# Kernel optimization log

Measured on AMD Instinct MI355X. Metric: run time of the kernel, lower is better.

The kernel has to match this reference:

```python
import jax, jax.numpy as jnp
import numpy as np

B, L, D_IN = 4, 2048, 80
D, H, DFF, WIN = 128, 16, 128, 64
DH = D // H
BN_EPS = 1e-5


def sinusoidal_positional_encoding(l, d, dtype):
    # Faithful to source: pos_j = 10000 ** (j / d) (exponent j/d, not 2j/d)
    n = d // 2 + (d % 2 == 1)
    pos_i = jnp.arange(l, dtype=dtype)[:, None]                  # [L,1]
    pos_j = jnp.power(jnp.asarray(10000.0, dtype), jnp.arange(n, dtype=dtype) / d)  # [n]
    ang = pos_i / pos_j                                          # [L,n]
    pos = jnp.stack([jnp.sin(ang), jnp.cos(ang)], axis=-1).reshape(l, -1)
    return pos[:, :d]                                            # [L,D]


def local_window_disallowed_mask(l, win):
    # Source: mask starts as ones (True = disallowed), zeros only strictly
    i = jnp.arange(l)
    diff = jnp.abs(i[:, None] - i[None, :])
    allowed = (diff >= 1) & (diff <= win)
    return ~allowed                                              # [L,L] bool, True = masked


def setup_inputs() -> dict:
    key = jax.random.key(0)
    ks = jax.random.split(key, 17)
    s = 0.05  # weight scale for numerical stability
    return {
        "x": jax.random.normal(ks[0], (B, L, D_IN), jnp.float32),
        "conv_w": jax.random.normal(ks[1], (D, D_IN), jnp.float32) * s,
        "conv_b": jax.random.normal(ks[2], (D,), jnp.float32) * s,
        "bn_g": jax.random.uniform(ks[3], (D,), jnp.float32, 0.5, 1.5),
        "bn_b": jax.random.normal(ks[4], (D,), jnp.float32) * s,
        "bn_rm": jax.random.normal(ks[5], (D,), jnp.float32) * s,
        "bn_rv": jax.random.uniform(ks[6], (D,), jnp.float32, 0.5, 1.5),
        "in_proj_w": jax.random.normal(ks[7], (3 * D, D), jnp.float32) * s,
        "in_proj_b": jax.random.normal(ks[8], (3 * D,), jnp.float32) * s,
        "out_w": jax.random.normal(ks[9], (D, D), jnp.float32) * s,
        "out_b": jax.random.normal(ks[10], (D,), jnp.float32) * s,
        "ff_w1": jax.random.normal(ks[11], (DFF, D), jnp.float32) * s,
        "ff_b1": jax.random.normal(ks[12], (DFF,), jnp.float32) * s,
        "ff_w2": jax.random.normal(ks[13], (D, DFF), jnp.float32) * s,
        "ff_b2": jax.random.normal(ks[14], (D,), jnp.float32) * s,
        "fc_w": jax.random.normal(ks[15], (D_IN, D), jnp.float32) * s,
        "fc_b": jax.random.normal(ks[16], (D_IN,), jnp.float32) * s,
    }


def _forward(x, conv_w, conv_b, bn_g, bn_b, bn_rm, bn_rv,
             in_proj_w, in_proj_b, out_w, out_b,
             ff_w1, ff_b1, ff_w2, ff_b2, fc_w, fc_b):
    b, l, _ = x.shape
    dt = x.dtype
    # Conv1d(kernel=1) + ReLU + BatchNorm1d (eval mode, running stats)
    h = jax.nn.relu(jnp.einsum('bli,oi->blo', x, conv_w) + conv_b)     # [B,L,D]
    h = (h - bn_rm) * (bn_g * jax.lax.rsqrt(bn_rv + BN_EPS)) + bn_b
    # positional encoding
    h = h + sinusoidal_positional_encoding(l, D, dt)
    # MultiheadAttention (torch semantics: joint in_proj, scaled dot, out_proj)
    qkv = jnp.einsum('bld,ed->ble', h, in_proj_w) + in_proj_b          # [B,L,3D]
    q, k, v = jnp.split(qkv, 3, axis=-1)
    q = q.reshape(b, l, H, DH).transpose(0, 2, 1, 3)                   # [B,H,L,dh]
    k = k.reshape(b, l, H, DH).transpose(0, 2, 1, 3)
    v = v.reshape(b, l, H, DH).transpose(0, 2, 1, 3)
    scores = jnp.einsum('bhqd,bhkd->bhqk', q, k) / jnp.sqrt(jnp.asarray(DH, dt))
    mask = local_window_disallowed_mask(l, WIN)                        # True = masked
    scores = jnp.where(mask, jnp.finfo(dt).min, scores)
    attn = jax.nn.softmax(scores, axis=-1)                             # [B,H,L,L]
    ctx = jnp.einsum('bhqk,bhkd->bhqd', attn, v)
    ctx = ctx.transpose(0, 2, 1, 3).reshape(b, l, D)
    attn_out = jnp.einsum('bld,od->blo', ctx, out_w) + out_b           # [B,L,D]
    # FFN (no residual in source)
    f = jax.nn.relu(jnp.einsum('bld,fd->blf', attn_out, ff_w1) + ff_b1)
    f = jnp.einsum('blf,df->bld', f, ff_w2) + ff_b2                    # [B,L,D]
    # final head
    return jnp.einsum('bld,od->blo', f, fc_w) + fc_b                   # [B,L,80]


def reference(x, conv_w, conv_b, bn_g, bn_b, bn_rm, bn_rv,
              in_proj_w, in_proj_b, out_w, out_b,
              ff_w1, ff_b1, ff_w2, ff_b2, fc_w, fc_b):
    return _forward(x, conv_w, conv_b, bn_g, bn_b, bn_rm, bn_rv,
                    in_proj_w, in_proj_b, out_w, out_b,
                    ff_w1, ff_b1, ff_w2, ff_b2, fc_w, fc_b)
```

## Files before the change

### kernel.cpp

```cpp
#include <hip/hip_runtime.h>
#include <math.h>

constexpr int L_ = 2048, D_ = 128, H_ = 16;
constexpr int T_ = 8192;
constexpr int LDX = T_;

typedef __attribute__((ext_vector_type(8))) short short8;
typedef __attribute__((ext_vector_type(4))) float floatx4;

__device__ unsigned short g_h_hi[T_ * D_];
__device__ unsigned short g_h_lo[T_ * D_];
__device__ unsigned short g_Wq_hi[3 * D_ * D_];
__device__ unsigned short g_Wq_lo[3 * D_ * D_];
__device__ float g_qkv [3 * D_ * T_];
__device__ unsigned short g_ctxH[T_ * D_];
__device__ unsigned short g_ctxL[T_ * D_];
__device__ unsigned short g_Mf1H[D_ * D_];
__device__ unsigned short g_Mf1L[D_ * D_];
__device__ unsigned short g_MfcH[D_ * D_];
__device__ unsigned short g_MfcL[D_ * D_];
__device__ float g_bf1 [D_];
__device__ float g_bfc [D_];

__device__ __forceinline__ unsigned short bf16h(float x) {
    unsigned u = __float_as_uint(x);
    return (unsigned short)((u + 0x7FFFu + ((u >> 16) & 1u)) >> 16);
}
__device__ __forceinline__ float bf16f(unsigned short h) {
    return __uint_as_float(((unsigned)h) << 16);
}

__global__ __launch_bounds__(256) void stage1_kernel(
        const float* __restrict__ x, const float* __restrict__ conv_w,
        const float* __restrict__ conv_b,
        const float* __restrict__ bg, const float* __restrict__ bb,
        const float* __restrict__ brm, const float* __restrict__ brv,
        const float* __restrict__ in_proj_w,
        const float* __restrict__ out_w,  const float* __restrict__ out_b,
        const float* __restrict__ ff_w1,  const float* __restrict__ ff_b1,
        const float* __restrict__ ff_w2,  const float* __restrict__ ff_b2,
        const float* __restrict__ fc_w,   const float* __restrict__ fc_b) {
    __shared__ unsigned short sm[2 * 32 * 104];
    int bid = blockIdx.x, tid = threadIdx.x;

    if (bid < 256) {
        unsigned short* XsH = sm;
        unsigned short* XsL = sm + 32 * 104;
        int t0 = bid * 32;

        for (int p = tid; p < 1280; p += 256) {
            int f0 = p * 2;
            int r = f0 / 80, k = f0 - r * 80;
            float2 v2 = *(const float2*)&x[(size_t)(t0 + r) * 80 + k];
            unsigned short h0 = bf16h(v2.x), h1 = bf16h(v2.y);
            *(unsigned*)&XsH[r * 104 + k] = (unsigned)h0 | ((unsigned)h1 << 16);
            *(unsigned*)&XsL[r * 104 + k] =
                (unsigned)bf16h(v2.x - bf16f(h0)) |
                ((unsigned)bf16h(v2.y - bf16f(h1)) << 16);
        }
        for (int i = tid; i < 384; i += 256) {
            int r = i / 12, k = 80 + 2 * (i - r * 12);
            *(unsigned*)&XsH[r * 104 + k] = 0u;
            *(unsigned*)&XsL[r * 104 + k] = 0u;
        }
        __syncthreads();

        int lane = tid & 63, w = tid >> 6;
        int m16 = lane & 15, quad = lane >> 4;

        short8 aH[2][3], aL[2][3];
#pragma unroll
        for (int mt = 0; mt < 2; mt++) {
            int c = w * 32 + mt * 16 + m16;
#pragma unroll
            for (int kt = 0; kt < 3; kt++) {
                int kb = kt * 32 + quad * 8;
                short8 vh = {0, 0, 0, 0, 0, 0, 0, 0};
                short8 vl = {0, 0, 0, 0, 0, 0, 0, 0};
                if (kb < 80) {
                    float4 f0 = *(const float4*)&conv_w[(size_t)c * 80 + kb];
                    float4 f1 = *(const float4*)&conv_w[(size_t)c * 80 + kb + 4];
                    float vv[8] = {f0.x, f0.y, f0.z, f0.w, f1.x, f1.y, f1.z, f1.w};
#pragma unroll
                    for (int e = 0; e < 8; e++) {
                        unsigned short hh = bf16h(vv[e]);
                        vh[e] = (short)hh;
                        vl[e] = (short)bf16h(vv[e] - bf16f(hh));
                    }
                }
                aH[mt][kt] = vh; aL[mt][kt] = vl;
            }
        }

#pragma unroll
        for (int mt = 0; mt < 2; mt++) {
#pragma unroll
            for (int nt = 0; nt < 2; nt++) {
                floatx4 acc = {0.f, 0.f, 0.f, 0.f};
                int trow = nt * 16 + m16;
#pragma unroll
                for (int kt = 0; kt < 3; kt++) {
                    short8 bHv = *(short8*)&XsH[trow * 104 + kt * 32 + quad * 8];
                    short8 bLv = *(short8*)&XsL[trow * 104 + kt * 32 + quad * 8];
                    acc = __builtin_amdgcn_mfma_f32_16x16x32_bf16(aH[mt][kt], bHv, acc, 0, 0, 0);
                    acc = __builtin_amdgcn_mfma_f32_16x16x32_bf16(aL[mt][kt], bHv, acc, 0, 0, 0);
                    acc = __builtin_amdgcn_mfma_f32_16x16x32_bf16(aH[mt][kt], bLv, acc, 0, 0, 0);
                }
                int c0 = w * 32 + mt * 16 + quad * 4;
                int t = t0 + nt * 16 + m16;
                int l = t & 2047;
                float vr[4];
#pragma unroll
                for (int r = 0; r < 4; r++) {
                    int c = c0 + r;
                    float v = acc[r] + conv_b[c];
                    v = fmaxf(v, 0.0f);
                    v = (v - brm[c]) * (bg[c] * rsqrtf(brv[c] + 1e-5f)) + bb[c];
                    float inv = __expf((float)(c >> 1) * (-9.210340371976184f / 128.0f));
                    float ang = (float)l * inv;
                    v += (c & 1) ? cosf(ang) : sinf(ang);
                    vr[r] = v;
                }
                unsigned short h0 = bf16h(vr[0]), h1 = bf16h(vr[1]);
                unsigned short h2 = bf16h(vr[2]), h3 = bf16h(vr[3]);
                unsigned hp[2] = {(unsigned)h0 | ((unsigned)h1 << 16),
                                  (unsigned)h2 | ((unsigned)h3 << 16)};
                unsigned lp[2] = {
                    (unsigned)bf16h(vr[0] - bf16f(h0)) | ((unsigned)bf16h(vr[1] - bf16f(h1)) << 16),
                    (unsigned)bf16h(vr[2] - bf16f(h2)) | ((unsigned)bf16h(vr[3] - bf16f(h3)) << 16)};
                *(uint2*)&g_h_hi[(size_t)t * 128 + c0] = *(uint2*)hp;
                *(uint2*)&g_h_lo[(size_t)t * 128 + c0] = *(uint2*)lp;
            }
        }
        return;
    }
    if (bid < 304) {
        int e4 = ((bid - 256) * 256 + tid) * 4;
        float4 v = *(const float4*)&in_proj_w[e4];
        float vv[4] = {v.x, v.y, v.z, v.w};
        unsigned short hh[4], ll[4];
#pragma unroll
        for (int e = 0; e < 4; e++) {
            hh[e] = bf16h(vv[e]);
            ll[e] = bf16h(vv[e] - bf16f(hh[e]));
        }
        unsigned hp[2] = {(unsigned)hh[0] | ((unsigned)hh[1] << 16),
                          (unsigned)hh[2] | ((unsigned)hh[3] << 16)};
        unsigned lp[2] = {(unsigned)ll[0] | ((unsigned)ll[1] << 16),
                          (unsigned)ll[2] | ((unsigned)ll[3] << 16)};
        *(uint2*)&g_Wq_hi[e4] = *(uint2*)hp;
        *(uint2*)&g_Wq_lo[e4] = *(uint2*)lp;
        return;
    }
    float* rowbuf = (float*)sm;
    float* red = (float*)sm + 256;
    if (bid < 368) {
        int sub = tid >> 7, k = tid & 127;
        int f = (bid - 304) * 2 + sub;
        rowbuf[sub * 128 + k] = ff_w1[f * 128 + k];
        __syncthreads();
        float acc = 0.f;
#pragma unroll 8
        for (int o = 0; o < 128; o++)
            acc = fmaf(rowbuf[sub * 128 + o], out_w[o * 128 + k], acc);
        unsigned short hi = bf16h(acc);
        g_Mf1H[f * 128 + k] = hi;
        g_Mf1L[f * 128 + k] = bf16h(acc - bf16f(hi));
        red[tid] = rowbuf[sub * 128 + k] * out_b[k];
        __syncthreads();
        for (int s = 64; s > 0; s >>= 1) {
            if (k < s) red[tid] += red[tid + s];
            __syncthreads();
        }
        if (k == 0) g_bf1[f] = red[sub * 128] + ff_b1[f];
        return;
    }
    {
        int sub = tid >> 7, k = tid & 127;
        int o = (bid - 368) * 2 + sub;
        rowbuf[sub * 128 + k] = (o < 80) ? fc_w[o * 128 + k] : 0.f;
        __syncthreads();
        float acc = 0.f;
#pragma unroll 8
        for (int d = 0; d < 128; d++)
            acc = fmaf(rowbuf[sub * 128 + d], ff_w2[d * 128 + k], acc);
        unsigned short hi = bf16h(acc);
        g_MfcH[o * 128 + k] = hi;
        g_MfcL[o * 128 + k] = bf16h(acc - bf16f(hi));
        red[tid] = rowbuf[sub * 128 + k] * ff_b2[k];
        __syncthreads();
        for (int s = 64; s > 0; s >>= 1) {
            if (k < s) red[tid] += red[tid + s];
            __syncthreads();
        }
        if (k == 0) g_bfc[o] = (o < 80) ? (red[sub * 128] + fc_b[o]) : 0.f;
        return;
    }
}

__global__ __launch_bounds__(256) void qkv_mfma(const float* __restrict__ in_proj_b) {
    __shared__ unsigned short WsH[64 * 136];
    __shared__ unsigned short WsL[64 * 136];
    __shared__ unsigned short HsH[32 * 136];
    __shared__ unsigned short HsL[32 * 136];
    int tid = threadIdx.x;
    int t0 = blockIdx.x * 32;
    int cb = blockIdx.y * 64;

    for (int i = tid; i < 1024; i += 256) {
        int r = i >> 4, c8 = (i & 15) * 8;
        *(uint4*)&WsH[r * 136 + c8] = *(const uint4*)&g_Wq_hi[(size_t)(cb + r) * 128 + c8];
        *(uint4*)&WsL[r * 136 + c8] = *(const uint4*)&g_Wq_lo[(size_t)(cb + r) * 128 + c8];
    }
    for (int i = tid; i < 512; i += 256) {
        int r = i >> 4, c8 = (i & 15) * 8;
        *(uint4*)&HsH[r * 136 + c8] = *(const uint4*)&g_h_hi[(size_t)(t0 + r) * 128 + c8];
        *(uint4*)&HsL[r * 136 + c8] = *(const uint4*)&g_h_lo[(size_t)(t0 + r) * 128 + c8];
    }
    __syncthreads();

    int lane = tid & 63, w = tid >> 6;
    int m16 = lane & 15, quad = lane >> 4;
    int c0 = w * 16;

    short8 aH[4], aL[4];
#pragma unroll
    for (int kt = 0; kt < 4; kt++) {
        aH[kt] = *(short8*)&WsH[(c0 + m16) * 136 + kt * 32 + quad * 8];
        aL[kt] = *(short8*)&WsL[(c0 + m16) * 136 + kt * 32 + quad * 8];
    }
    float bias_r[4];
#pragma unroll
    for (int r = 0; r < 4; r++) bias_r[r] = in_proj_b[cb + c0 + quad * 4 + r];

#pragma unroll
    for (int s = 0; s < 2; s++) {
        floatx4 acc = {0.f, 0.f, 0.f, 0.f};
        int trow = s * 16 + m16;
#pragma unroll
        for (int kt = 0; kt < 4; kt++) {
            short8 bH = *(short8*)&HsH[trow * 136 + kt * 32 + quad * 8];
            short8 bL = *(short8*)&HsL[trow * 136 + kt * 32 + quad * 8];
            acc = __builtin_amdgcn_mfma_f32_16x16x32_bf16(aH[kt], bH, acc, 0, 0, 0);
            acc = __builtin_amdgcn_mfma_f32_16x16x32_bf16(aL[kt], bH, acc, 0, 0, 0);
            acc = __builtin_amdgcn_mfma_f32_16x16x32_bf16(aH[kt], bL, acc, 0, 0, 0);
        }
#pragma unroll
        for (int r = 0; r < 4; r++)
            g_qkv[(size_t)(cb + c0 + quad * 4 + r) * LDX + t0 + s * 16 + m16] =
                acc[r] + bias_r[r];
    }
}

__global__ __launch_bounds__(256) void attn_kernel() {
    __shared__ float4 SK[2][2][324];
    __shared__ float4 SV[2][2][324];
    int bh = blockIdx.x;
    int qb = blockIdx.y * 512;
    int b = bh >> 4, h = bh & 15;
    int tb = b * L_;
    int tid = threadIdx.x;
    int jbase = qb - 64;

    for (int c16 = 0; c16 < 16; c16++) {
        int d = c16 & 7;
        int ch = ((c16 < 8) ? D_ : 2 * D_) + h * 8 + d;
        const float* src = g_qkv + (size_t)ch * LDX + tb;
        float4* base4 = ((c16 < 8) ? &SK[0][0][0] : &SV[0][0][0]) + (d >> 2) * 324;
        for (int s = tid; s < 641; s += 256) {
            int j = jbase + s;
            float v = ((unsigned)j < (unsigned)L_) ? src[j] : 0.f;
            ((float*)(base4 + (s & 1) * 648 + (s >> 1)))[d & 3] = v;
        }
    }
    __syncthreads();

    const float sc = 0.35355339059327373f;
    int q0 = qb + 2 * tid;
    float qa[8], qc[8];
#pragma unroll
    for (int d = 0; d < 8; d++) {
        qa[d] = g_qkv[(size_t)(h * 8 + d) * LDX + tb + q0] * sc;
        qc[d] = g_qkv[(size_t)(h * 8 + d) * LDX + tb + q0 + 1] * sc;
    }
    float l0 = 0.f, l1 = 0.f;
    float A0[8] = {}, A1[8] = {};
    int j00 = jbase + 2 * tid;

#pragma unroll 2
    for (int it = 0; it <= 129; it++) {
        int pp = it & 1, idx = tid + (it >> 1);
        float4 ka = SK[pp][0][idx], kb2 = SK[pp][1][idx];
        float kv[8] = {ka.x, ka.y, ka.z, ka.w, kb2.x, kb2.y, kb2.z, kb2.w};
        float s0 = 0.f, s1 = 0.f;
#pragma unroll
        for (int d = 0; d < 8; d++) {
            s0 = fmaf(qa[d], kv[d], s0);
            s1 = fmaf(qc[d], kv[d], s1);
        }
        bool jv = (unsigned)(j00 + it) < (unsigned)L_;
        float w0 = (jv && it != 64 && it <= 128) ? __expf(s0) : 0.f;
        float w1 = (jv && it != 65 && it >= 1)  ? __expf(s1) : 0.f;
        l0 += w0; l1 += w1;
        float4 va = SV[pp][0][idx], vb2 = SV[pp][1][idx];
        float vv[8] = {va.x, va.y, va.z, va.w, vb2.x, vb2.y, vb2.z, vb2.w};
#pragma unroll
        for (int d = 0; d < 8; d++) {
            A0[d] = fmaf(w0, vv[d], A0[d]);
            A1[d] = fmaf(w1, vv[d], A1[d]);
        }
    }
    float i0 = 1.f / l0, i1 = 1.f / l1;
    unsigned hp[4], lp[4];
#pragma unroll
    for (int d2 = 0; d2 < 4; d2++) {
        float v0 = A0[2 * d2] * i0, v1 = A0[2 * d2 + 1] * i0;
        unsigned short h0 = bf16h(v0), h1 = bf16h(v1);
        hp[d2] = (unsigned)h0 | ((unsigned)h1 << 16);
        lp[d2] = (unsigned)bf16h(v0 - bf16f(h0)) |
                 ((unsigned)bf16h(v1 - bf16f(h1)) << 16);
    }
    *(uint4*)&g_ctxH[(size_t)(tb + q0) * 128 + h * 8] = *(uint4*)hp;
    *(uint4*)&g_ctxL[(size_t)(tb + q0) * 128 + h * 8] = *(uint4*)lp;
#pragma unroll
    for (int d2 = 0; d2 < 4; d2++) {
        float v0 = A1[2 * d2] * i1, v1 = A1[2 * d2 + 1] * i1;
        unsigned short h0 = bf16h(v0), h1 = bf16h(v1);
        hp[d2] = (unsigned)h0 | ((unsigned)h1 << 16);
        lp[d2] = (unsigned)bf16h(v0 - bf16f(h0)) |
                 ((unsigned)bf16h(v1 - bf16f(h1)) << 16);
    }
    *(uint4*)&g_ctxH[(size_t)(tb + q0 + 1) * 128 + h * 8] = *(uint4*)hp;
    *(uint4*)&g_ctxL[(size_t)(tb + q0 + 1) * 128 + h * 8] = *(uint4*)lp;
}

__global__ __launch_bounds__(256) void f1fc_mfma(float* __restrict__ out) {
    __shared__ unsigned short sm[4 * 32 * 136];
    unsigned short* ctxH = sm;
    unsigned short* ctxL = sm + 32 * 136;
    unsigned short* C1H  = sm + 2 * 32 * 136;
    unsigned short* C1L  = sm + 3 * 32 * 136;
    float* C2 = (float*)sm;
    __shared__ float b1s[128];

    int tid = threadIdx.x;
    int t0 = blockIdx.x * 32;

    for (int i = tid; i < 512; i += 256) {
        int r = i >> 4, c8 = (i & 15) * 8;
        *(uint4*)&ctxH[r * 136 + c8] = *(const uint4*)&g_ctxH[(size_t)(t0 + r) * 128 + c8];
        *(uint4*)&ctxL[r * 136 + c8] = *(const uint4*)&g_ctxL[(size_t)(t0 + r) * 128 + c8];
    }
    if (tid < 128) b1s[tid] = g_bf1[tid];
    __syncthreads();

    int lane = tid & 63, w = tid >> 6;
    int m16 = lane & 15, quad = lane >> 4;

    floatx4 acc1[2][2];
#pragma unroll
    for (int mt = 0; mt < 2; mt++) {
        int fbase = w * 32 + mt * 16 + m16;
        short8 aH[4], aL[4];
#pragma unroll
        for (int kt = 0; kt < 4; kt++) {
            aH[kt] = *(const short8*)&g_Mf1H[(size_t)fbase * 128 + kt * 32 + quad * 8];
            aL[kt] = *(const short8*)&g_Mf1L[(size_t)fbase * 128 + kt * 32 + quad * 8];
        }
#pragma unroll
        for (int nt = 0; nt < 2; nt++) {
            floatx4 acc = {0.f, 0.f, 0.f, 0.f};
            int trow = nt * 16 + m16;
#pragma unroll
            for (int kt = 0; kt < 4; kt++) {
                short8 bH = *(short8*)&ctxH[trow * 136 + kt * 32 + quad * 8];
                short8 bL = *(short8*)&ctxL[trow * 136 + kt * 32 + quad * 8];
                acc = __builtin_amdgcn_mfma_f32_16x16x32_bf16(aH[kt], bH, acc, 0, 0, 0);
                acc = __builtin_amdgcn_mfma_f32_16x16x32_bf16(aL[kt], bH, acc, 0, 0, 0);
                acc = __builtin_amdgcn_mfma_f32_16x16x32_bf16(aH[kt], bL, acc, 0, 0, 0);
            }
            acc1[mt][nt] = acc;
        }
    }
#pragma unroll
    for (int mt = 0; mt < 2; mt++) {
#pragma unroll
        for (int nt = 0; nt < 2; nt++) {
            int f0 = w * 32 + mt * 16 + quad * 4;
            int t = nt * 16 + m16;
            float v[4];
#pragma unroll
            for (int r = 0; r < 4; r++)
                v[r] = fmaxf(acc1[mt][nt][r] + b1s[f0 + r], 0.f);
            unsigned short h0 = bf16h(v[0]), h1 = bf16h(v[1]);
            unsigned short h2 = bf16h(v[2]), h3 = bf16h(v[3]);
            *(unsigned*)&C1H[t * 136 + f0]     = (unsigned)h0 | ((unsigned)h1 << 16);
            *(unsigned*)&C1H[t * 136 + f0 + 2] = (unsigned)h2 | ((unsigned)h3 << 16);
            *(unsigned*)&C1L[t * 136 + f0] =
                (unsigned)bf16h(v[0] - bf16f(h0)) | ((unsigned)bf16h(v[1] - bf16f(h1)) << 16);
            *(unsigned*)&C1L[t * 136 + f0 + 2] =
                (unsigned)bf16h(v[2] - bf16f(h2)) | ((unsigned)bf16h(v[3] - bf16f(h3)) << 16);
        }
    }
    __syncthreads();

    floatx4 acc2[2][2];
#pragma unroll
    for (int mt = 0; mt < 2; mt++) {
        int obase = w * 32 + mt * 16 + m16;
        short8 aH[4], aL[4];
#pragma unroll
        for (int kt = 0; kt < 4; kt++) {
            aH[kt] = *(const short8*)&g_MfcH[(size_t)obase * 128 + kt * 32 + quad * 8];
            aL[kt] = *(const short8*)&g_MfcL[(size_t)obase * 128 + kt * 32 + quad * 8];
        }
#pragma unroll
        for (int nt = 0; nt < 2; nt++) {
            floatx4 acc = {0.f, 0.f, 0.f, 0.f};
            int trow = nt * 16 + m16;
#pragma unroll
            for (int kt = 0; kt < 4; kt++) {
                short8 bH = *(short8*)&C1H[trow * 136 + kt * 32 + quad * 8];
                short8 bL = *(short8*)&C1L[trow * 136 + kt * 32 + quad * 8];
                acc = __builtin_amdgcn_mfma_f32_16x16x32_bf16(aH[kt], bH, acc, 0, 0, 0);
                acc = __builtin_amdgcn_mfma_f32_16x16x32_bf16(aL[kt], bH, acc, 0, 0, 0);
                acc = __builtin_amdgcn_mfma_f32_16x16x32_bf16(aH[kt], bL, acc, 0, 0, 0);
            }
            acc2[mt][nt] = acc;
        }
    }
    __syncthreads();
#pragma unroll
    for (int mt = 0; mt < 2; mt++) {
        int o0 = w * 32 + mt * 16 + quad * 4;
        if (o0 < 96) {
#pragma unroll
            for (int nt = 0; nt < 2; nt++) {
                int t = nt * 16 + m16;
#pragma unroll
                for (int r = 0; r < 4; r++)
                    C2[t * 100 + o0 + r] = acc2[mt][nt][r] + g_bfc[o0 + r];
            }
        }
    }
    __syncthreads();
    for (int i = tid; i < 640; i += 256) {
        int t = i / 20, c4 = i - t * 20;
        *(float4*)&out[(size_t)(t0 + t) * 80 + c4 * 4] = *(float4*)&C2[t * 100 + c4 * 4];
    }
}

extern "C" void kernel_launch(void* const* d_in, const int* in_sizes, int n_in,
                              void* d_out, int out_size, void* d_ws, size_t ws_size,
                              hipStream_t stream) {
    const float* x         = (const float*)d_in[0];
    const float* conv_w    = (const float*)d_in[1];
    const float* conv_b    = (const float*)d_in[2];
    const float* bn_g      = (const float*)d_in[3];
    const float* bn_b      = (const float*)d_in[4];
    const float* bn_rm     = (const float*)d_in[5];
    const float* bn_rv     = (const float*)d_in[6];
    const float* in_proj_w = (const float*)d_in[7];
    const float* in_proj_b = (const float*)d_in[8];
    const float* out_w     = (const float*)d_in[9];
    const float* out_b     = (const float*)d_in[10];
    const float* ff_w1     = (const float*)d_in[11];
    const float* ff_b1     = (const float*)d_in[12];
    const float* ff_w2     = (const float*)d_in[13];
    const float* ff_b2     = (const float*)d_in[14];
    const float* fc_w      = (const float*)d_in[15];
    const float* fc_b      = (const float*)d_in[16];

    stage1_kernel<<<432, 256, 0, stream>>>(x, conv_w, conv_b, bn_g, bn_b,
                                           bn_rm, bn_rv, in_proj_w,
                                           out_w, out_b, ff_w1, ff_b1,
                                           ff_w2, ff_b2, fc_w, fc_b);

    qkv_mfma<<<dim3(256, 6), 256, 0, stream>>>(in_proj_b);

    attn_kernel<<<dim3(64, 4), 256, 0, stream>>>();

    f1fc_mfma<<<256, 256, 0, stream>>>((float*)d_out);
}
```

Before: 146.7 us.

## Fuse QKV projection into stage1 conv kernel, keeping h in shared memory

The conv/BN/positional-encoding output tile now goes to shared memory instead of global bf16 hi/lo buffers. The same block then runs the QKV projection with MFMA, splitting in_proj_w into bf16 hi/lo in registers on the fly. This removes one kernel launch, the global round trip of h, and the separate weight-conversion blocks. In exchange, each of the 256 blocks reloads and converts the full 384x128 fp32 weight matrix and does six times the MFMA work serially, so there is less parallelism than the previous 1536-block QKV grid.

After: 146.8 us (median of 2 runs). About the same (+0.0%).

```diff
diff --git a/kernel.cpp b/kernel.cpp
--- a/kernel.cpp
+++ b/kernel.cpp
@@ -8,10 +8,6 @@
 typedef __attribute__((ext_vector_type(8))) short short8;
 typedef __attribute__((ext_vector_type(4))) float floatx4;
 
-__device__ unsigned short g_h_hi[T_ * D_];
-__device__ unsigned short g_h_lo[T_ * D_];
-__device__ unsigned short g_Wq_hi[3 * D_ * D_];
-__device__ unsigned short g_Wq_lo[3 * D_ * D_];
 __device__ float g_qkv [3 * D_ * T_];
 __device__ unsigned short g_ctxH[T_ * D_];
 __device__ unsigned short g_ctxL[T_ * D_];
@@ -35,17 +31,19 @@
         const float* __restrict__ conv_b,
         const float* __restrict__ bg, const float* __restrict__ bb,
         const float* __restrict__ brm, const float* __restrict__ brv,
-        const float* __restrict__ in_proj_w,
+        const float* __restrict__ in_proj_w, const float* __restrict__ in_proj_b,
         const float* __restrict__ out_w,  const float* __restrict__ out_b,
         const float* __restrict__ ff_w1,  const float* __restrict__ ff_b1,
         const float* __restrict__ ff_w2,  const float* __restrict__ ff_b2,
         const float* __restrict__ fc_w,   const float* __restrict__ fc_b) {
-    __shared__ unsigned short sm[2 * 32 * 104];
+    __shared__ unsigned short sm[15360];
+    unsigned short* XsH = sm;
+    unsigned short* XsL = sm + 3328;
+    unsigned short* HsH = sm + 6656;
+    unsigned short* HsL = sm + 11008;
     int bid = blockIdx.x, tid = threadIdx.x;
 
     if (bid < 256) {
-        unsigned short* XsH = sm;
-        unsigned short* XsL = sm + 32 * 104;
         int t0 = bid * 32;
 
         for (int p = tid; p < 1280; p += 256) {
@@ -128,35 +126,61 @@
                 unsigned lp[2] = {
                     (unsigned)bf16h(vr[0] - bf16f(h0)) | ((unsigned)bf16h(vr[1] - bf16f(h1)) << 16),
                     (unsigned)bf16h(vr[2] - bf16f(h2)) | ((unsigned)bf16h(vr[3] - bf16f(h3)) << 16)};
-                *(uint2*)&g_h_hi[(size_t)t * 128 + c0] = *(uint2*)hp;
-                *(uint2*)&g_h_lo[(size_t)t * 128 + c0] = *(uint2*)lp;
-            }
-        }
-        return;
-    }
-    if (bid < 304) {
-        int e4 = ((bid - 256) * 256 + tid) * 4;
-        float4 v = *(const float4*)&in_proj_w[e4];
-        float vv[4] = {v.x, v.y, v.z, v.w};
-        unsigned short hh[4], ll[4];
-#pragma unroll
-        for (int e = 0; e < 4; e++) {
-            hh[e] = bf16h(vv[e]);
-            ll[e] = bf16h(vv[e] - bf16f(hh[e]));
-        }
-        unsigned hp[2] = {(unsigned)hh[0] | ((unsigned)hh[1] << 16),
-                          (unsigned)hh[2] | ((unsigned)hh[3] << 16)};
-        unsigned lp[2] = {(unsigned)ll[0] | ((unsigned)ll[1] << 16),
-                          (unsigned)ll[2] | ((unsigned)ll[3] << 16)};
-        *(uint2*)&g_Wq_hi[e4] = *(uint2*)hp;
-        *(uint2*)&g_Wq_lo[e4] = *(uint2*)lp;
+                int tl = nt * 16 + m16;
+                *(uint2*)&HsH[tl * 136 + c0] = *(uint2*)hp;
+                *(uint2*)&HsL[tl * 136 + c0] = *(uint2*)lp;
+            }
+        }
+        __syncthreads();
+
+#pragma unroll
+        for (int ti = 0; ti < 6; ti++) {
+            int c0 = w * 96 + ti * 16;
+            short8 wH[4], wL[4];
+#pragma unroll
+            for (int kt = 0; kt < 4; kt++) {
+                int kb = kt * 32 + quad * 8;
+                float4 f0 = *(const float4*)&in_proj_w[(size_t)(c0 + m16) * 128 + kb];
+                float4 f1 = *(const float4*)&in_proj_w[(size_t)(c0 + m16) * 128 + kb + 4];
+                float vv[8] = {f0.x, f0.y, f0.z, f0.w, f1.x, f1.y, f1.z, f1.w};
+                short8 vh, vl;
+#pragma unroll
+                for (int e = 0; e < 8; e++) {
+                    unsigned short hh = bf16h(vv[e]);
+                    vh[e] = (short)hh;
+                    vl[e] = (short)bf16h(vv[e] - bf16f(hh));
+                }
+                wH[kt] = vh; wL[kt] = vl;
+            }
+            float bias_r[4];
+#pragma unroll
+            for (int r = 0; r < 4; r++) bias_r[r] = in_proj_b[c0 + quad * 4 + r];
+
+#pragma unroll
+            for (int s = 0; s < 2; s++) {
+                floatx4 acc = {0.f, 0.f, 0.f, 0.f};
+                int trow = s * 16 + m16;
+#pragma unroll
+                for (int kt = 0; kt < 4; kt++) {
+                    short8 bH = *(short8*)&HsH[trow * 136 + kt * 32 + quad * 8];
+                    short8 bL = *(short8*)&HsL[trow * 136 + kt * 32 + quad * 8];
+                    acc = __builtin_amdgcn_mfma_f32_16x16x32_bf16(wH[kt], bH, acc, 0, 0, 0);
+                    acc = __builtin_amdgcn_mfma_f32_16x16x32_bf16(wL[kt], bH, acc, 0, 0, 0);
+                    acc = __builtin_amdgcn_mfma_f32_16x16x32_bf16(wH[kt], bL, acc, 0, 0, 0);
+                }
+#pragma unroll
+                for (int r = 0; r < 4; r++)
+                    g_qkv[(size_t)(c0 + quad * 4 + r) * LDX + t0 + s * 16 + m16] =
+                        acc[r] + bias_r[r];
+            }
+        }
         return;
     }
     float* rowbuf = (float*)sm;
     float* red = (float*)sm + 256;
-    if (bid < 368) {
+    if (bid < 320) {
         int sub = tid >> 7, k = tid & 127;
-        int f = (bid - 304) * 2 + sub;
+        int f = (bid - 256) * 2 + sub;
         rowbuf[sub * 128 + k] = ff_w1[f * 128 + k];
         __syncthreads();
         float acc = 0.f;
@@ -177,7 +201,7 @@
     }
     {
         int sub = tid >> 7, k = tid & 127;
-        int o = (bid - 368) * 2 + sub;
+        int o = (bid - 320) * 2 + sub;
         rowbuf[sub * 128 + k] = (o < 80) ? fc_w[o * 128 + k] : 0.f;
         __syncthreads();
         float acc = 0.f;
@@ -195,60 +219,6 @@
         }
         if (k == 0) g_bfc[o] = (o < 80) ? (red[sub * 128] + fc_b[o]) : 0.f;
         return;
-    }
-}
-
-__global__ __launch_bounds__(256) void qkv_mfma(const float* __restrict__ in_proj_b) {
-    __shared__ unsigned short WsH[64 * 136];
-    __shared__ unsigned short WsL[64 * 136];
-    __shared__ unsigned short HsH[32 * 136];
-    __shared__ unsigned short HsL[32 * 136];
-    int tid = threadIdx.x;
-    int t0 = blockIdx.x * 32;
-    int cb = blockIdx.y * 64;
-
-    for (int i = tid; i < 1024; i += 256) {
-        int r = i >> 4, c8 = (i & 15) * 8;
-        *(uint4*)&WsH[r * 136 + c8] = *(const uint4*)&g_Wq_hi[(size_t)(cb + r) * 128 + c8];
-        *(uint4*)&WsL[r * 136 + c8] = *(const uint4*)&g_Wq_lo[(size_t)(cb + r) * 128 + c8];
-    }
-    for (int i = tid; i < 512; i += 256) {
-        int r = i >> 4, c8 = (i & 15) * 8;
-        *(uint4*)&HsH[r * 136 + c8] = *(const uint4*)&g_h_hi[(size_t)(t0 + r) * 128 + c8];
-        *(uint4*)&HsL[r * 136 + c8] = *(const uint4*)&g_h_lo[(size_t)(t0 + r) * 128 + c8];
-    }
-    __syncthreads();
-
-    int lane = tid & 63, w = tid >> 6;
-    int m16 = lane & 15, quad = lane >> 4;
-    int c0 = w * 16;
-
-    short8 aH[4], aL[4];
-#pragma unroll
-    for (int kt = 0; kt < 4; kt++) {
-        aH[kt] = *(short8*)&WsH[(c0 + m16) * 136 + kt * 32 + quad * 8];
-        aL[kt] = *(short8*)&WsL[(c0 + m16) * 136 + kt * 32 + quad * 8];
-    }
-    float bias_r[4];
-#pragma unroll
-    for (int r = 0; r < 4; r++) bias_r[r] = in_proj_b[cb + c0 + quad * 4 + r];
-
-#pragma unroll
-    for (int s = 0; s < 2; s++) {
-        floatx4 acc = {0.f, 0.f, 0.f, 0.f};
-        int trow = s * 16 + m16;
-#pragma unroll
-        for (int kt = 0; kt < 4; kt++) {
-            short8 bH = *(short8*)&HsH[trow * 136 + kt * 32 + quad * 8];
-            short8 bL = *(short8*)&HsL[trow * 136 + kt * 32 + quad * 8];
-            acc = __builtin_amdgcn_mfma_f32_16x16x32_bf16(aH[kt], bH, acc, 0, 0, 0);
-            acc = __builtin_amdgcn_mfma_f32_16x16x32_bf16(aL[kt], bH, acc, 0, 0, 0);
-            acc = __builtin_amdgcn_mfma_f32_16x16x32_bf16(aH[kt], bL, acc, 0, 0, 0);
-        }
-#pragma unroll
-        for (int r = 0; r < 4; r++)
-            g_qkv[(size_t)(cb + c0 + quad * 4 + r) * LDX + t0 + s * 16 + m16] =
-                acc[r] + bias_r[r];
     }
 }
 
@@ -471,13 +441,11 @@
     const float* fc_w      = (const float*)d_in[15];
     const float* fc_b      = (const float*)d_in[16];
 
-    stage1_kernel<<<432, 256, 0, stream>>>(x, conv_w, conv_b, bn_g, bn_b,
-                                           bn_rm, bn_rv, in_proj_w,
+    stage1_kernel<<<384, 256, 0, stream>>>(x, conv_w, conv_b, bn_g, bn_b,
+                                           bn_rm, bn_rv, in_proj_w, in_proj_b,
                                            out_w, out_b, ff_w1, ff_b1,
                                            ff_w2, ff_b2, fc_w, fc_b);
 
-    qkv_mfma<<<dim3(256, 6), 256, 0, stream>>>(in_proj_b);
-
     attn_kernel<<<dim3(64, 4), 256, 0, stream>>>();
 
     f1fc_mfma<<<256, 256, 0, stream>>>((float*)d_out);
```
